# Kernel optimization log

Measured on AMD Instinct MI355X. Metric: run time of the kernel, lower is better.

Reference implementation:

```python
import jax, jax.numpy as jnp
import numpy as np

B, S, D, H = 4, 4096, 256, 4
Dh = D // H


def setup_inputs() -> dict:
    key = jax.random.key(0)
    ks = jax.random.split(key, 5)
    scale = 1.0 / np.sqrt(D)
    return {
        "inputs": jax.random.normal(ks[0], (B, S, D), dtype=jnp.float32),
        "Wq": jax.random.normal(ks[1], (D, D), dtype=jnp.float32) * scale,
        "bq": jnp.zeros((D,), jnp.float32),
        "Wk": jax.random.normal(ks[2], (D, D), dtype=jnp.float32) * scale,
        "bk": jnp.zeros((D,), jnp.float32),
        "Wv": jax.random.normal(ks[3], (D, D), dtype=jnp.float32) * scale,
        "bv": jnp.zeros((D,), jnp.float32),
        "Wo": jax.random.normal(ks[4], (D, D), dtype=jnp.float32) * scale,
        "bo": jnp.zeros((D,), jnp.float32),
    }


def reference(inputs, Wq, bq, Wk, bk, Wv, bv, Wo, bo):
    b, s, d = inputs.shape
    # QKV projections
    q = inputs @ Wq + bq
    k = inputs @ Wk + bk
    v = inputs @ Wv + bv
    # separate heads: [B, S, D] -> [B, H, S, Dh]
    def split_heads(x):
        return x.reshape(b, s, H, Dh).transpose(0, 2, 1, 3)
    q, k, v = split_heads(q), split_heads(k), split_heads(v)
    # scaled dot-product attention (no causal mask: mask=False)
    scores = jnp.einsum("bhqd,bhkd->bhqk", q, k) / jnp.sqrt(jnp.float32(Dh))
    weights = jax.nn.softmax(scores, axis=-1)
    attn = jnp.einsum("bhqk,bhkd->bhqd", weights, v)
    # combine heads: [B, H, S, Dh] -> [B, S, D]
    attn = attn.transpose(0, 2, 1, 3).reshape(b, s, d)
    return attn @ Wo + bo
```

## Files before the change

kernel.cpp:

```cpp
#include <hip/hip_runtime.h>
#include <cmath>

#define B_  4
#define S_  4096
#define D_  256
#define H_  4
#define DH_ 64
#define M_TOTAL (B_*S_)
#define QSCALE 0.1803368801111f

typedef __bf16 bf16x8 __attribute__((ext_vector_type(8)));
typedef __bf16 bf16x4 __attribute__((ext_vector_type(4)));
typedef __bf16 bf16x2 __attribute__((ext_vector_type(2)));
typedef float  f32x4  __attribute__((ext_vector_type(4)));
typedef float  f32x16 __attribute__((ext_vector_type(16)));

#define AS1 __attribute__((address_space(1)))
#define AS3 __attribute__((address_space(3)))

__device__ __forceinline__ void g2lds16(const void* g, void* l) {
    __builtin_amdgcn_global_load_lds((AS1 const void*)g, (AS3 void*)l, 16, 0, 0);
}

#if __has_builtin(__builtin_amdgcn_permlane32_swap)
typedef unsigned uint2v __attribute__((ext_vector_type(2)));
__device__ __forceinline__ void plswap(unsigned &a, unsigned &b) {
    uint2v r = __builtin_amdgcn_permlane32_swap(a, b, false, false);
    a = r[0]; b = r[1];
}
#else
__device__ __forceinline__ void plswap(unsigned &a, unsigned &b) {
    unsigned bl = (unsigned)__shfl_xor((int)b, 32);
    unsigned ah = (unsigned)__shfl_xor((int)a, 32);
    bool hi = (threadIdx.x & 32) != 0;
    unsigned na = hi ? bl : a;
    unsigned nb = hi ? b  : ah;
    a = na; b = nb;
}
#endif

__device__ __forceinline__ unsigned pk2(float x, float y) {
    bf16x2 t; t[0] = (__bf16)x; t[1] = (__bf16)y;
    return __builtin_bit_cast(unsigned, t);
}

__global__ __launch_bounds__(256) void prep(const float* __restrict__ X,
                                            const float* __restrict__ W0,
                                            const float* __restrict__ W1,
                                            const float* __restrict__ W2,
                                            const float* __restrict__ W3,
                                            __bf16* __restrict__ Xb,
                                            __bf16* __restrict__ Wt_all) {
    int t = threadIdx.x;
    if (blockIdx.x < 2048) {
        size_t i = ((size_t)blockIdx.x * 256 + t) * 8;
        float4 v0 = *(const float4*)(X + i);
        float4 v1 = *(const float4*)(X + i + 4);
        bf16x8 o;
        o[0] = (__bf16)v0.x; o[1] = (__bf16)v0.y; o[2] = (__bf16)v0.z; o[3] = (__bf16)v0.w;
        o[4] = (__bf16)v1.x; o[5] = (__bf16)v1.y; o[6] = (__bf16)v1.z; o[7] = (__bf16)v1.w;
        *(bf16x8*)(Xb + i) = o;
        return;
    }
    int bid = blockIdx.x - 2048;
    int z = bid >> 6, rem = bid & 63;
    int by = rem >> 3, bx = rem & 7;
    const float* W = (z == 0) ? W0 : (z == 1) ? W1 : (z == 2) ? W2 : W3;
    float wsc = (z == 0) ? QSCALE : 1.0f;
    __bf16* Wt = Wt_all + (size_t)z * 65536;
    __shared__ float tile[32][33];
    int r0 = by * 32, c0 = bx * 32;
#pragma unroll
    for (int e = 0; e < 4; e++) {
        int idx = t + e * 256; int r = idx >> 5, c = idx & 31;
        tile[r][c] = W[(r0 + r) * 256 + c0 + c];
    }
    __syncthreads();
#pragma unroll
    for (int e = 0; e < 4; e++) {
        int idx = t + e * 256; int r = idx >> 5, c = idx & 31;
        Wt[(c0 + r) * 256 + (r0 + c)] = (__bf16)(tile[c][r] * wsc);
    }
}

__global__ __launch_bounds__(256) void gemm_bt(const __bf16* __restrict__ A,
                                               const __bf16* __restrict__ Wt_all,
                                               const float* __restrict__ bias0,
                                               const float* __restrict__ bias1,
                                               const float* __restrict__ bias2,
                                               __bf16* __restrict__ outb,
                                               __bf16* __restrict__ voutb,
                                               float* __restrict__ outf,
                                               int out_is_f32, float bsc0) {
    constexpr int K = 256;
    __shared__ __attribute__((aligned(16))) __bf16 As[128 * 32];
    __shared__ __attribute__((aligned(16))) __bf16 Bs[128 * 32];

    int t = threadIdx.x;
    int lane = t & 63, w = t >> 6;
    int wr = w >> 1, wc = w & 1;
    int l16 = lane & 15, quad = lane >> 4;
    int mbase = blockIdx.x * 128;
    int nbase = blockIdx.y * 128;
    int z = blockIdx.z;
    const __bf16* Bt = Wt_all + (size_t)z * 65536;
    const float* bias = (z == 0) ? bias0 : (z == 1) ? bias1 : bias2;
    float bscale = (z == 0) ? bsc0 : 1.0f;

    f32x4 acc[4][4] = {};

    int srow = t >> 2;
    int sseg = (t & 3) * 8;

    for (int kk = 0; kk < K; kk += 32) {
        __syncthreads();
        g2lds16(A  + (size_t)(mbase +      srow) * K + kk + sseg, (char*)As +        t * 16);
        g2lds16(A  + (size_t)(mbase + 64 + srow) * K + kk + sseg, (char*)As + 4096 + t * 16);
        g2lds16(Bt + (size_t)(nbase +      srow) * K + kk + sseg, (char*)Bs +        t * 16);
        g2lds16(Bt + (size_t)(nbase + 64 + srow) * K + kk + sseg, (char*)Bs + 4096 + t * 16);
        __syncthreads();

        bf16x8 a[4], b[4];
#pragma unroll
        for (int i = 0; i < 4; i++)
            a[i] = *(const bf16x8*)(As + (wr * 64 + i * 16 + l16) * 32 + quad * 8);
#pragma unroll
        for (int j = 0; j < 4; j++)
            b[j] = *(const bf16x8*)(Bs + (wc * 64 + j * 16 + l16) * 32 + quad * 8);
#pragma unroll
        for (int i = 0; i < 4; i++)
#pragma unroll
            for (int j = 0; j < 4; j++)
                acc[i][j] = __builtin_amdgcn_mfma_f32_16x16x32_bf16(a[i], b[j], acc[i][j], 0, 0, 0);
    }

#pragma unroll
    for (int i = 0; i < 4; i++) {
#pragma unroll
        for (int j = 0; j < 4; j++) {
            int col = nbase + wc * 64 + j * 16 + l16;
            float bv = bias[col] * bscale;
            int row0 = mbase + wr * 64 + i * 16 + quad * 4;
            if (out_is_f32) {
#pragma unroll
                for (int r = 0; r < 4; r++)
                    outf[(size_t)(row0 + r) * 256 + col] = acc[i][j][r] + bv;
            } else if (z == 2) {
                int hcol = col >> 6, dh = col & 63;
                int bidx = row0 >> 12, s0 = row0 & 4095;
                bf16x4 pk;
#pragma unroll
                for (int r = 0; r < 4; r++) pk[r] = (__bf16)(acc[i][j][r] + bv);
                *(bf16x4*)(voutb + ((size_t)(bidx * 4 + hcol) * 64 + dh) * 4096 + s0) = pk;
            } else {
#pragma unroll
                for (int r = 0; r < 4; r++)
                    outb[(size_t)z * ((size_t)M_TOTAL * 256) + (size_t)(row0 + r) * 256 + col] =
                        (__bf16)(acc[i][j][r] + bv);
            }
        }
    }
}

__global__ __launch_bounds__(256, 2) void attn(const __bf16* __restrict__ Qb,
                                               const __bf16* __restrict__ Kb,
                                               const __bf16* __restrict__ Vt,
                                               __bf16* __restrict__ Ctx) {
    __shared__ __attribute__((aligned(16))) __bf16 smem[32768];

    int t = threadIdx.x;
    int lane = t & 63, w = t >> 6;
    int l31 = lane & 31, hh = lane >> 5;
    int kw = w & 1, qw2 = w >> 1;

    int lin = blockIdx.x;
    int xcd = lin & 7, j = lin >> 3;
    int bh = xcd * 2 + (j & 1);
    int qblk = j >> 1;
    int b = bh >> 2, hd = bh & 3;
    int qw = qblk * 128 + qw2 * 64;

    const __bf16* Kbase = Kb + (size_t)b * S_ * 256 + hd * 64;
    const __bf16* Vbase = Vt + (size_t)bh * 64 * S_;

    bf16x8 qf[4][2];
#pragma unroll
    for (int ks = 0; ks < 4; ks++)
#pragma unroll
        for (int qt = 0; qt < 2; qt++)
            qf[ks][qt] = *(const bf16x8*)(Qb + (size_t)(b * S_ + qw + qt * 32 + l31) * 256
                                              + hd * 64 + ks * 16 + hh * 8);

    f32x16 acc[2][2] = {};
    float lsum[2] = {0.f, 0.f};

    int srow = t >> 3;
    int sseg = t & 7;

#define STAGE(kv, slot) do {                                                   \
        char* mk = (char*)smem + (slot) * 16384;                               \
        char* mv = mk + 8192;                                                  \
        _Pragma("unroll")                                                      \
        for (int c = 0; c < 2; c++) {                                          \
            int rr = c * 32 + srow;                                            \
            int gseg = (sseg ^ (rr & 7)) * 8;                                  \
            g2lds16(Kbase + (size_t)((kv) + rr) * 256 + gseg,                  \
                    mk + c * 4096 + t * 16);                                   \
            g2lds16(Vbase + (size_t)rr * S_ + (kv) + gseg,                     \
                    mv + c * 4096 + t * 16);                                   \
        }                                                                      \
    } while (0)

#define QKSTEP(TILE, SN) do {                                                  \
        __bf16* Ksp = (__bf16*)((char*)smem + ((TILE) & 3) * 16384);           \
        bf16x8 kfv[4];                                                         \
        _Pragma("unroll")                                                      \
        for (int ks = 0; ks < 4; ks++) {                                       \
            int slot = (ks * 2 + hh) ^ (l31 & 7);                              \
            kfv[ks] = *(const bf16x8*)(Ksp + (kw * 32 + l31) * 64 + slot * 8); \
        }                                                                      \
        _Pragma("unroll")                                                      \
        for (int qt = 0; qt < 2; qt++) SN[qt] = (f32x16){};                    \
        _Pragma("unroll")                                                      \
        for (int ks = 0; ks < 4; ks++)                                         \
            _Pragma("unroll")                                                  \
            for (int qt = 0; qt < 2; qt++)                                     \
                SN[qt] = __builtin_amdgcn_mfma_f32_32x32x16_bf16(              \
                    kfv[ks], qf[ks][qt], SN[qt], 0, 0, 0);                     \
    } while (0)

#define SMPV(IT, SC) do {                                                      \
        __bf16* Vsp = (__bf16*)((char*)smem + ((IT) & 3) * 16384) + 4096;      \
        unsigned dd[2][8];                                                     \
        _Pragma("unroll")                                                      \
        for (int qt = 0; qt < 2; qt++) {                                       \
            float p[16];                                                       \
            _Pragma("unroll")                                                  \
            for (int r = 0; r < 16; r++)                                       \
                p[r] = __builtin_amdgcn_exp2f(SC[qt][r]);                      \
            float s0 = ((p[0]+p[1])+(p[2]+p[3]))+((p[4]+p[5])+(p[6]+p[7]));    \
            float s1 = ((p[8]+p[9])+(p[10]+p[11]))+((p[12]+p[13])+(p[14]+p[15])); \
            lsum[qt] += s0 + s1;                                               \
            _Pragma("unroll")                                                  \
            for (int m = 0; m < 4; m++) {                                      \
                dd[qt][m*2]   = pk2(p[4*m],   p[4*m+1]);                       \
                dd[qt][m*2+1] = pk2(p[4*m+2], p[4*m+3]);                       \
            }                                                                  \
        }                                                                      \
        _Pragma("unroll")                                                      \
        for (int tt = 0; tt < 2; tt++) {                                       \
            int tks = kw * 2 + tt;                                             \
            bf16x8 pf[2];                                                      \
            _Pragma("unroll")                                                  \
            for (int qt = 0; qt < 2; qt++) {                                   \
                unsigned x0 = dd[qt][4*tt],   y0 = dd[qt][4*tt+2];             \
                unsigned x1 = dd[qt][4*tt+1], y1 = dd[qt][4*tt+3];             \
                plswap(x0, y0);                                                \
                plswap(x1, y1);                                                \
                union { unsigned u[4]; bf16x8 v; } c;                          \
                c.u[0] = x0; c.u[1] = x1; c.u[2] = y0; c.u[3] = y1;            \
                pf[qt] = c.v;                                                  \
            }                                                                  \
            _Pragma("unroll")                                                  \
            for (int mt = 0; mt < 2; mt++) {                                   \
                int slot = (tks * 2 + hh) ^ (l31 & 7);                         \
                bf16x8 vf = *(const bf16x8*)(Vsp + (mt*32 + l31)*64 + slot*8); \
                _Pragma("unroll")                                              \
                for (int qt = 0; qt < 2; qt++)                                 \
                    acc[mt][qt] = __builtin_amdgcn_mfma_f32_32x32x16_bf16(     \
                        vf, pf[qt], acc[mt][qt], 0, 0, 0);                     \
            }                                                                  \
        }                                                                      \
    } while (0)

#define BODY(IT, SC, SN) do {                                                  \
        if ((IT) < 62) asm volatile("s_waitcnt vmcnt(4)" ::: "memory");        \
        else           asm volatile("s_waitcnt vmcnt(0)" ::: "memory");        \
        asm volatile("s_barrier" ::: "memory");                                \
        if ((IT) <= 60) STAGE(((IT) + 3) * 64, ((IT) + 3) & 3);                \
        if ((IT) < 63) QKSTEP((IT) + 1, SN);                                   \
        SMPV(IT, SC);                                                          \
    } while (0)

    f32x16 stA[2], stB[2];

    STAGE(0, 0);
    STAGE(64, 1);
    STAGE(128, 2);
    asm volatile("s_waitcnt vmcnt(8)" ::: "memory");
    asm volatile("s_barrier" ::: "memory");
    QKSTEP(0, stA);

    for (int it = 0; it < 64; it += 2) {
        BODY(it,     stA, stB);
        BODY(it + 1, stB, stA);
    }
#undef BODY
#undef SMPV
#undef QKSTEP
#undef STAGE

#pragma unroll
    for (int qt = 0; qt < 2; qt++)
        lsum[qt] += __shfl_xor(lsum[qt], 32);

    __syncthreads();
    float* lsd = (float*)((char*)smem + 32768);
    if (kw == 1) {
#pragma unroll
        for (int mt = 0; mt < 2; mt++)
#pragma unroll
            for (int qt = 0; qt < 2; qt++)
#pragma unroll
                for (int g = 0; g < 4; g++) {
                    f32x4 v;
#pragma unroll
                    for (int e = 0; e < 4; e++) v[e] = acc[mt][qt][4 * g + e];
                    *(f32x4*)((char*)smem + qw2 * 16384
                              + ((mt * 2 + qt) * 4 + g) * 1024 + lane * 16) = v;
                }
        lsd[qw2 * 128 + lane * 2 + 0] = lsum[0];
        lsd[qw2 * 128 + lane * 2 + 1] = lsum[1];
    }
    __syncthreads();
    if (kw == 0) {
        float inv[2];
#pragma unroll
        for (int qt = 0; qt < 2; qt++)
            inv[qt] = 1.f / (lsum[qt] + lsd[qw2 * 128 + lane * 2 + qt]);
#pragma unroll
        for (int mt = 0; mt < 2; mt++)
#pragma unroll
            for (int qt = 0; qt < 2; qt++)
#pragma unroll
                for (int g = 0; g < 4; g++) {
                    f32x4 v = *(const f32x4*)((char*)smem + qw2 * 16384
                                              + ((mt * 2 + qt) * 4 + g) * 1024 + lane * 16);
#pragma unroll
                    for (int e = 0; e < 4; e++) acc[mt][qt][4 * g + e] += v[e];
                }

        __bf16* Es = smem + 18432 + qw2 * 4608;
#pragma unroll
        for (int qt = 0; qt < 2; qt++)
#pragma unroll
            for (int mt = 0; mt < 2; mt++)
#pragma unroll
                for (int rg = 0; rg < 4; rg++) {
                    bf16x4 ov;
#pragma unroll
                    for (int e = 0; e < 4; e++)
                        ov[e] = (__bf16)(acc[mt][qt][4 * rg + e] * inv[qt]);
                    int dhb = mt * 32 + rg * 8 + 4 * hh;
                    *(bf16x4*)(Es + (qt * 32 + l31) * 72 + dhb) = ov;
                }
#pragma unroll
        for (int pass = 0; pass < 8; pass++) {
            int q = pass * 8 + (lane >> 3);
            int col = (lane & 7) * 8;
            bf16x8 val = *(const bf16x8*)(Es + q * 72 + col);
            *(bf16x8*)(Ctx + (size_t)(b * S_ + qw + q) * 256 + hd * 64 + col) = val;
        }
    }
}

extern "C" void kernel_launch(void* const* d_in, const int* in_sizes, int n_in,
                              void* d_out, int out_size, void* d_ws, size_t ws_size,
                              hipStream_t stream) {
    const float* X  = (const float*)d_in[0];
    const float* Wq = (const float*)d_in[1];
    const float* bq = (const float*)d_in[2];
    const float* Wk = (const float*)d_in[3];
    const float* bk = (const float*)d_in[4];
    const float* Wv = (const float*)d_in[5];
    const float* bv = (const float*)d_in[6];
    const float* Wo = (const float*)d_in[7];
    const float* bo = (const float*)d_in[8];
    float* out = (float*)d_out;

    char* ws = (char*)d_ws;
    const size_t MB = 1024 * 1024;
    __bf16* Xb  = (__bf16*)(ws);
    __bf16* Ctx = (__bf16*)(ws);
    __bf16* Wt  = (__bf16*)(ws + 8 * MB);
    __bf16* Qb  = (__bf16*)(ws + 8 * MB + 512 * 1024);
    __bf16* Kb  = (__bf16*)((char*)Qb + 8 * MB);
    __bf16* Vt  = (__bf16*)((char*)Kb + 8 * MB);

    prep<<<dim3(2304), dim3(256), 0, stream>>>(X, Wq, Wk, Wv, Wo, Xb, Wt);
    gemm_bt<<<dim3(M_TOTAL / 128, 2, 3), dim3(256), 0, stream>>>(
        Xb, Wt, bq, bk, bv, Qb, Vt, nullptr, 0, QSCALE);
    attn<<<dim3(512), dim3(256), 0, stream>>>(Qb, Kb, Vt, Ctx);
    gemm_bt<<<dim3(M_TOTAL / 128, 2, 1), dim3(256), 0, stream>>>(
        Ctx, Wt + 3 * 65536, bo, bo, bo, nullptr, nullptr, out, 1, 1.0f);
}
```

Baseline: 177.2 us.

## Pre-swizzle K and V into MFMA fragment order and load directly from global

The projection GEMM now writes K and V in a layout that already matches the per-lane MFMA operand fragments. The attention kernel drops its LDS staging, barriers and swizzled LDS reads, and instead loads K and V fragments straight from global memory into registers, prefetching K two tiles ahead. This removes LDS traffic and block-wide synchronisation. In exchange, global load latency is exposed inside the loop, V prefetch happens only one step ahead, and register pressure rises. The K epilogue also switches to scattered scalar bf16 stores.

```diff
diff --git a/kernel.cpp b/kernel.cpp
--- a/kernel.cpp
+++ b/kernel.cpp
@@ -89,6 +89,7 @@
                                                const float* __restrict__ bias1,
                                                const float* __restrict__ bias2,
                                                __bf16* __restrict__ outb,
+                                               __bf16* __restrict__ koutb,
                                                __bf16* __restrict__ voutb,
                                                float* __restrict__ outf,
                                                int out_is_f32, float bsc0) {
@@ -146,25 +147,40 @@
                 for (int r = 0; r < 4; r++)
                     outf[(size_t)(row0 + r) * 256 + col] = acc[i][j][r] + bv;
             } else if (z == 2) {
-                int hcol = col >> 6, dh = col & 63;
+                int hd = col >> 6, dh = col & 63;
+                int mt = dh >> 5, l31v = dh & 31;
                 int bidx = row0 >> 12, s0 = row0 & 4095;
+                int tile = s0 >> 6, tks = (s0 >> 4) & 3, hhk = (s0 >> 3) & 1;
+                int bh2 = bidx * 4 + hd;
+                size_t addr = ((((size_t)bh2 * 64 + tile) * 4 + tks) * 2 + mt) * 512
+                              + (hhk * 32 + l31v) * 8 + (s0 & 7);
                 bf16x4 pk;
 #pragma unroll
                 for (int r = 0; r < 4; r++) pk[r] = (__bf16)(acc[i][j][r] + bv);
-                *(bf16x4*)(voutb + ((size_t)(bidx * 4 + hcol) * 64 + dh) * 4096 + s0) = pk;
+                *(bf16x4*)(voutb + addr) = pk;
+            } else if (z == 1) {
+                int hd = col >> 6, n6 = col & 63;
+                int ks = (n6 >> 4) & 3, hhq = (n6 >> 3) & 1, e = n6 & 7;
+                int bidx = row0 >> 12, s0 = row0 & 4095;
+                int tile = s0 >> 6, kwv = (s0 >> 5) & 1, l31k = s0 & 31;
+                int bh2 = bidx * 4 + hd;
+                size_t addr = ((((size_t)bh2 * 64 + tile) * 2 + kwv) * 4 + ks) * 512
+                              + (hhq * 32 + l31k) * 8 + e;
+#pragma unroll
+                for (int r = 0; r < 4; r++)
+                    koutb[addr + (size_t)r * 8] = (__bf16)(acc[i][j][r] + bv);
             } else {
 #pragma unroll
                 for (int r = 0; r < 4; r++)
-                    outb[(size_t)z * ((size_t)M_TOTAL * 256) + (size_t)(row0 + r) * 256 + col] =
-                        (__bf16)(acc[i][j][r] + bv);
+                    outb[(size_t)(row0 + r) * 256 + col] = (__bf16)(acc[i][j][r] + bv);
             }
         }
     }
 }
 
 __global__ __launch_bounds__(256, 2) void attn(const __bf16* __restrict__ Qb,
-                                               const __bf16* __restrict__ Kb,
-                                               const __bf16* __restrict__ Vt,
+                                               const __bf16* __restrict__ Kf,
+                                               const __bf16* __restrict__ Vf,
                                                __bf16* __restrict__ Ctx) {
     __shared__ __attribute__((aligned(16))) __bf16 smem[32768];
 
@@ -180,8 +196,8 @@
     int b = bh >> 2, hd = bh & 3;
     int qw = qblk * 128 + qw2 * 64;
 
-    const __bf16* Kbase = Kb + (size_t)b * S_ * 256 + hd * 64;
-    const __bf16* Vbase = Vt + (size_t)bh * 64 * S_;
+    const __bf16* Kbh = Kf + (size_t)bh * 262144;
+    const __bf16* Vbh = Vf + (size_t)bh * 262144;
 
     bf16x8 qf[4][2];
 #pragma unroll
@@ -194,31 +210,24 @@
     f32x16 acc[2][2] = {};
     float lsum[2] = {0.f, 0.f};
 
-    int srow = t >> 3;
-    int sseg = t & 7;
-
-#define STAGE(kv, slot) do {                                                   \
-        char* mk = (char*)smem + (slot) * 16384;                               \
-        char* mv = mk + 8192;                                                  \
-        _Pragma("unroll")                                                      \
-        for (int c = 0; c < 2; c++) {                                          \
-            int rr = c * 32 + srow;                                            \
-            int gseg = (sseg ^ (rr & 7)) * 8;                                  \
-            g2lds16(Kbase + (size_t)((kv) + rr) * 256 + gseg,                  \
-                    mk + c * 4096 + t * 16);                                   \
-            g2lds16(Vbase + (size_t)rr * S_ + (kv) + gseg,                     \
-                    mv + c * 4096 + t * 16);                                   \
-        }                                                                      \
+    int kw4 = kw * 4;
+    int kw2 = kw * 2;
+
+#define KLOAD(TILE, KF) do {                                                   \
+        const __bf16* Kp = Kbh + ((TILE) * 8 + kw4) * 512 + lane * 8;          \
+        _Pragma("unroll")                                                      \
+        for (int ks = 0; ks < 4; ks++)                                         \
+            KF[ks] = *(const bf16x8*)(Kp + ks * 512);                          \
     } while (0)
 
-#define QKSTEP(TILE, SN) do {                                                  \
-        __bf16* Ksp = (__bf16*)((char*)smem + ((TILE) & 3) * 16384);           \
-        bf16x8 kfv[4];                                                         \
-        _Pragma("unroll")                                                      \
-        for (int ks = 0; ks < 4; ks++) {                                       \
-            int slot = (ks * 2 + hh) ^ (l31 & 7);                              \
-            kfv[ks] = *(const bf16x8*)(Ksp + (kw * 32 + l31) * 64 + slot * 8); \
-        }                                                                      \
+#define VLOAD(TILE, VV) do {                                                   \
+        const __bf16* Vp = Vbh + (TILE) * 4096 + kw2 * 1024 + lane * 8;        \
+        _Pragma("unroll")                                                      \
+        for (int tm = 0; tm < 4; tm++)                                         \
+            VV[tm] = *(const bf16x8*)(Vp + tm * 512);                          \
+    } while (0)
+
+#define QKMFMA(KF, SN) do {                                                    \
         _Pragma("unroll")                                                      \
         for (int qt = 0; qt < 2; qt++) SN[qt] = (f32x16){};                    \
         _Pragma("unroll")                                                      \
@@ -226,11 +235,10 @@
             _Pragma("unroll")                                                  \
             for (int qt = 0; qt < 2; qt++)                                     \
                 SN[qt] = __builtin_amdgcn_mfma_f32_32x32x16_bf16(              \
-                    kfv[ks], qf[ks][qt], SN[qt], 0, 0, 0);                     \
+                    KF[ks], qf[ks][qt], SN[qt], 0, 0, 0);                      \
     } while (0)
 
-#define SMPV(IT, SC) do {                                                      \
-        __bf16* Vsp = (__bf16*)((char*)smem + ((IT) & 3) * 16384) + 4096;      \
+#define SMPV(SC, VV) do {                                                      \
         unsigned dd[2][8];                                                     \
         _Pragma("unroll")                                                      \
         for (int qt = 0; qt < 2; qt++) {                                       \
@@ -249,7 +257,6 @@
         }                                                                      \
         _Pragma("unroll")                                                      \
         for (int tt = 0; tt < 2; tt++) {                                       \
-            int tks = kw * 2 + tt;                                             \
             bf16x8 pf[2];                                                      \
             _Pragma("unroll")                                                  \
             for (int qt = 0; qt < 2; qt++) {                                   \
@@ -263,8 +270,7 @@
             }                                                                  \
             _Pragma("unroll")                                                  \
             for (int mt = 0; mt < 2; mt++) {                                   \
-                int slot = (tks * 2 + hh) ^ (l31 & 7);                         \
-                bf16x8 vf = *(const bf16x8*)(Vsp + (mt*32 + l31)*64 + slot*8); \
+                bf16x8 vf = VV[tt * 2 + mt];                                   \
                 _Pragma("unroll")                                              \
                 for (int qt = 0; qt < 2; qt++)                                 \
                     acc[mt][qt] = __builtin_amdgcn_mfma_f32_32x32x16_bf16(     \
@@ -273,32 +279,30 @@
         }                                                                      \
     } while (0)
 
-#define BODY(IT, SC, SN) do {                                                  \
-        if ((IT) < 62) asm volatile("s_waitcnt vmcnt(4)" ::: "memory");        \
-        else           asm volatile("s_waitcnt vmcnt(0)" ::: "memory");        \
-        asm volatile("s_barrier" ::: "memory");                                \
-        if ((IT) <= 60) STAGE(((IT) + 3) * 64, ((IT) + 3) & 3);                \
-        if ((IT) < 63) QKSTEP((IT) + 1, SN);                                   \
-        SMPV(IT, SC);                                                          \
+#define BODY(IT, SC, SN, KC, KN) do {                                          \
+        if ((IT) < 62) KLOAD((IT) + 2, KN);                                    \
+        bf16x8 vfv[4];                                                         \
+        VLOAD(IT, vfv);                                                        \
+        if ((IT) < 63) QKMFMA(KC, SN);                                         \
+        SMPV(SC, vfv);                                                         \
     } while (0)
 
+    bf16x8 kfA[4], kfB[4];
     f32x16 stA[2], stB[2];
 
-    STAGE(0, 0);
-    STAGE(64, 1);
-    STAGE(128, 2);
-    asm volatile("s_waitcnt vmcnt(8)" ::: "memory");
-    asm volatile("s_barrier" ::: "memory");
-    QKSTEP(0, stA);
+    KLOAD(0, kfA);
+    KLOAD(1, kfB);
+    QKMFMA(kfA, stA);
 
     for (int it = 0; it < 64; it += 2) {
-        BODY(it,     stA, stB);
-        BODY(it + 1, stB, stA);
+        BODY(it,     stA, stB, kfB, kfA);
+        BODY(it + 1, stB, stA, kfA, kfB);
     }
 #undef BODY
 #undef SMPV
-#undef QKSTEP
-#undef STAGE
+#undef QKMFMA
+#undef VLOAD
+#undef KLOAD
 
 #pragma unroll
     for (int qt = 0; qt < 2; qt++)
@@ -384,13 +388,13 @@
     __bf16* Ctx = (__bf16*)(ws);
     __bf16* Wt  = (__bf16*)(ws + 8 * MB);
     __bf16* Qb  = (__bf16*)(ws + 8 * MB + 512 * 1024);
-    __bf16* Kb  = (__bf16*)((char*)Qb + 8 * MB);
-    __bf16* Vt  = (__bf16*)((char*)Kb + 8 * MB);
+    __bf16* Kf  = (__bf16*)((char*)Qb + 8 * MB);
+    __bf16* Vf  = (__bf16*)((char*)Kf + 8 * MB);
 
     prep<<<dim3(2304), dim3(256), 0, stream>>>(X, Wq, Wk, Wv, Wo, Xb, Wt);
     gemm_bt<<<dim3(M_TOTAL / 128, 2, 3), dim3(256), 0, stream>>>(
-        Xb, Wt, bq, bk, bv, Qb, Vt, nullptr, 0, QSCALE);
-    attn<<<dim3(512), dim3(256), 0, stream>>>(Qb, Kb, Vt, Ctx);
+        Xb, Wt, bq, bk, bv, Qb, Kf, Vf, nullptr, 0, QSCALE);
+    attn<<<dim3(512), dim3(256), 0, stream>>>(Qb, Kf, Vf, Ctx);
     gemm_bt<<<dim3(M_TOTAL / 128, 2, 1), dim3(256), 0, stream>>>(
-        Ctx, Wt + 3 * 65536, bo, bo, bo, nullptr, nullptr, out, 1, 1.0f);
-}
+        Ctx, Wt + 3 * 65536, bo, bo, bo, nullptr, nullptr, nullptr, out, 1, 1.0f);
+}
```

After: 186.3 us. +5.1%, slower.

## Triple-buffer LDS tiles in projection GEMM to overlap global loads with MFMA

Applied to the files above, without the earlier changes.

Converts the QKV/output projection GEMM main loop from load-sync-compute into a 3-stage ring of LDS buffers. Loads for step s+2 are issued while step s computes, and explicit vmcnt waits with raw s_barrier replace the two __syncthreads per iteration. The goal is to hide global-to-LDS latency behind the MFMA work. In exchange, LDS use per block triples to 48KB, and occupancy is hinted at 3 blocks per CU through launch_bounds.

```diff
diff --git a/kernel.cpp b/kernel.cpp
--- a/kernel.cpp
+++ b/kernel.cpp
@@ -83,18 +83,18 @@
     }
 }
 
-__global__ __launch_bounds__(256) void gemm_bt(const __bf16* __restrict__ A,
-                                               const __bf16* __restrict__ Wt_all,
-                                               const float* __restrict__ bias0,
-                                               const float* __restrict__ bias1,
-                                               const float* __restrict__ bias2,
-                                               __bf16* __restrict__ outb,
-                                               __bf16* __restrict__ voutb,
-                                               float* __restrict__ outf,
-                                               int out_is_f32, float bsc0) {
+__global__ __launch_bounds__(256, 3) void gemm_bt(const __bf16* __restrict__ A,
+                                                  const __bf16* __restrict__ Wt_all,
+                                                  const float* __restrict__ bias0,
+                                                  const float* __restrict__ bias1,
+                                                  const float* __restrict__ bias2,
+                                                  __bf16* __restrict__ outb,
+                                                  __bf16* __restrict__ voutb,
+                                                  float* __restrict__ outf,
+                                                  int out_is_f32, float bsc0) {
     constexpr int K = 256;
-    __shared__ __attribute__((aligned(16))) __bf16 As[128 * 32];
-    __shared__ __attribute__((aligned(16))) __bf16 Bs[128 * 32];
+    __shared__ __attribute__((aligned(16))) __bf16 As[3 * 4096];
+    __shared__ __attribute__((aligned(16))) __bf16 Bs[3 * 4096];
 
     int t = threadIdx.x;
     int lane = t & 63, w = t >> 6;
@@ -112,27 +112,45 @@
     int srow = t >> 2;
     int sseg = (t & 3) * 8;
 
-    for (int kk = 0; kk < K; kk += 32) {
-        __syncthreads();
-        g2lds16(A  + (size_t)(mbase +      srow) * K + kk + sseg, (char*)As +        t * 16);
-        g2lds16(A  + (size_t)(mbase + 64 + srow) * K + kk + sseg, (char*)As + 4096 + t * 16);
-        g2lds16(Bt + (size_t)(nbase +      srow) * K + kk + sseg, (char*)Bs +        t * 16);
-        g2lds16(Bt + (size_t)(nbase + 64 + srow) * K + kk + sseg, (char*)Bs + 4096 + t * 16);
-        __syncthreads();
+#define GSTAGE(kk, slot) do {                                                  \
+        g2lds16(A  + (size_t)(mbase +      srow) * K + (kk) + sseg,            \
+                (char*)As + (slot) * 8192 +        t * 16);                    \
+        g2lds16(A  + (size_t)(mbase + 64 + srow) * K + (kk) + sseg,            \
+                (char*)As + (slot) * 8192 + 4096 + t * 16);                    \
+        g2lds16(Bt + (size_t)(nbase +      srow) * K + (kk) + sseg,            \
+                (char*)Bs + (slot) * 8192 +        t * 16);                    \
+        g2lds16(Bt + (size_t)(nbase + 64 + srow) * K + (kk) + sseg,            \
+                (char*)Bs + (slot) * 8192 + 4096 + t * 16);                    \
+    } while (0)
+
+    GSTAGE(0, 0);
+    GSTAGE(32, 1);
+
+    int rs = 0, ps = 2;
+#pragma unroll 1
+    for (int s = 0; s < 8; s++) {
+        if (s < 7) asm volatile("s_waitcnt vmcnt(4)" ::: "memory");
+        else       asm volatile("s_waitcnt vmcnt(0)" ::: "memory");
+        asm volatile("s_barrier" ::: "memory");
+        if (s < 6) GSTAGE((s + 2) * 32, ps);
 
         bf16x8 a[4], b[4];
 #pragma unroll
         for (int i = 0; i < 4; i++)
-            a[i] = *(const bf16x8*)(As + (wr * 64 + i * 16 + l16) * 32 + quad * 8);
+            a[i] = *(const bf16x8*)(As + rs * 4096 + (wr * 64 + i * 16 + l16) * 32 + quad * 8);
 #pragma unroll
         for (int j = 0; j < 4; j++)
-            b[j] = *(const bf16x8*)(Bs + (wc * 64 + j * 16 + l16) * 32 + quad * 8);
+            b[j] = *(const bf16x8*)(Bs + rs * 4096 + (wc * 64 + j * 16 + l16) * 32 + quad * 8);
 #pragma unroll
         for (int i = 0; i < 4; i++)
 #pragma unroll
             for (int j = 0; j < 4; j++)
                 acc[i][j] = __builtin_amdgcn_mfma_f32_16x16x32_bf16(a[i], b[j], acc[i][j], 0, 0, 0);
-    }
+
+        rs = (rs == 2) ? 0 : rs + 1;
+        ps = (ps == 2) ? 0 : ps + 1;
+    }
+#undef GSTAGE
 
 #pragma unroll
     for (int i = 0; i < 4; i++) {
```

Measured after the change: 180.6 us. No clear change (+1.9%).
